# Optimization experiments

Hardware: AMD Instinct MI355X
Metric: run time of the kernel (lower is better)

## Reference

```python
import jax, jax.numpy as jnp
import numpy as np

B, N, D, H = 32, 8192, 128, 128


def setup_inputs() -> dict:
    key = jax.random.key(0)
    ks = jax.random.split(key, 9)
    s = lambda k, shp, fan: jax.random.normal(k, shp, jnp.float32) / np.sqrt(fan)
    return {
        "x": jax.random.normal(ks[0], (B, N, D), jnp.float32),
        "Wg1": s(ks[1], (D, H), D), "bg1": jnp.zeros((H,), jnp.float32),
        "Wg2": s(ks[2], (H, 1), H), "bg2": jnp.zeros((1,), jnp.float32),
        "Wn1": s(ks[3], (D, H), D), "bn1": jnp.zeros((H,), jnp.float32),
        "Wn2": s(ks[4], (H, H), H), "bn2": jnp.zeros((H,), jnp.float32),
    }


def reference(x, Wg1, bg1, Wg2, bg2, Wn1, bn1, Wn2, bn2):
    # gate_nn: Linear -> SiLU -> Linear(->1); scores per node
    gate = jnp.einsum("bnd,dh->bnh", x, Wg1) + bg1
    gate = jax.nn.silu(gate)
    gate = jnp.einsum("bnh,ho->bno", gate, Wg2) + bg2  # [B,N,1]
    # nn: Linear -> SiLU -> Linear; transformed node features
    h = jax.nn.silu(jnp.einsum("bnd,dh->bnh", x, Wn1) + bn1)
    h = jnp.einsum("bnh,hk->bnk", h, Wn2) + bn2  # [B,N,H]
    # segment softmax over nodes of each graph (segments == batch dim here)
    attn = jax.nn.softmax(gate, axis=1)  # [B,N,1]
    # weighted-sum pooling per graph
    return jnp.sum(attn * h, axis=1)  # [B,H]
```

## Files before the change

kernel.cpp:

```cpp
#include <hip/hip_runtime.h>

#define B_ 32
#define N_ 8192
#define D_ 128
#define H_ 128
#define R_ (B_ * N_)

typedef _Float16 f16;
typedef __attribute__((ext_vector_type(4))) _Float16 f16x4;
typedef __attribute__((ext_vector_type(8))) _Float16 f16x8;
typedef __attribute__((ext_vector_type(4))) float f32x4;

static constexpr size_t HWS_OFF   = 0;
static constexpr size_t WPACK_OFF = (size_t)R_ * 128 * 2;
static constexpr size_t GWS_OFF   = WPACK_OFF + 3 * 128 * 128 * 2;
static constexpr size_t MX_OFF    = GWS_OFF + (size_t)R_ * 4;
static constexpr size_t INV_OFF   = MX_OFF + 32 * 4;

__device__ __forceinline__ float silu_f(float v) {
    return v / (1.0f + __expf(-v));
}

__device__ __forceinline__ f32x4 mfma16(f16x8 a, f16x8 b, f32x4 c) {
    return __builtin_amdgcn_mfma_f32_16x16x32_f16(a, b, c, 0, 0, 0);
}

__global__ void k0_prepack(const float* __restrict__ Wg1,
                           const float* __restrict__ Wn1,
                           const float* __restrict__ Wn2,
                           f16* __restrict__ wp) {
    int tid = blockIdx.x * 256 + threadIdx.x;
    int m    = tid >> 14;
    int r    = tid & 16383;
    int j    = r & 7;
    int lane = (r >> 3) & 63;
    int kc   = (r >> 9) & 3;
    int nt   = r >> 11;
    int k = kc * 32 + (lane >> 4) * 8 + j;
    int n = nt * 16 + (lane & 15);
    const float* W = (m == 0) ? Wg1 : (m == 1) ? Wn1 : Wn2;
    wp[tid] = (f16)W[k * 128 + n];
}

__global__ __launch_bounds__(512) void k1_fused_gemm(
        const float* __restrict__ x,
        const float* __restrict__ bg1, const float* __restrict__ wg2,
        const float* __restrict__ bg2,
        const float* __restrict__ bn1, const float* __restrict__ bn2,
        const f16* __restrict__ wp,
        f16* __restrict__ hws, float* __restrict__ gws) {
    __shared__ f16 xlds[64 * 136];
    __shared__ f16 h1lds[64 * 136];
    __shared__ float gpart[8][64];

    const int tid  = threadIdx.x;
    const int w    = tid >> 6;
    const int lane = tid & 63;
    const int q    = lane >> 4;
    const int c    = lane & 15;
    const int colg = w * 16 + c;

    const f16x8* wpv = (const f16x8*)wp;
    f16x8 fg1[4], fn1[4], fn2[4];
#pragma unroll
    for (int kc = 0; kc < 4; ++kc) {
        int base = (w * 4 + kc) * 64 + lane;
        fg1[kc] = wpv[base];
        fn1[kc] = wpv[2048 + base];
        fn2[kc] = wpv[4096 + base];
    }
    const float bg1v = bg1[colg];
    const float bn1v = bn1[colg];
    const float bn2v = bn2[colg];
    const float wg2v = wg2[colg];
    const float bg2v = bg2[0];

    for (int it = 0; it < 8; ++it) {
        const long tile = (long)blockIdx.x * 8 + it;
        const long tb   = tile * 64;

        __syncthreads();

        const float4* xg = ((const float4*)x) + tb * 32;
#pragma unroll
        for (int s = 0; s < 4; ++s) {
            int i   = s * 512 + tid;
            int row = i >> 5;
            int c4  = i & 31;
            float4 v = xg[i];
            f16x4 hv = {(f16)v.x, (f16)v.y, (f16)v.z, (f16)v.w};
            *(f16x4*)&xlds[row * 136 + c4 * 4] = hv;
        }
        __syncthreads();

#pragma unroll
        for (int mt = 0; mt < 4; ++mt) {
            f16x8 a[4];
            const int arow = mt * 16 + c;
#pragma unroll
            for (int kc = 0; kc < 4; ++kc)
                a[kc] = *(const f16x8*)&xlds[arow * 136 + kc * 32 + q * 8];

            f32x4 ag = {0.f, 0.f, 0.f, 0.f};
            f32x4 an = {0.f, 0.f, 0.f, 0.f};
#pragma unroll
            for (int kc = 0; kc < 4; ++kc) {
                ag = mfma16(a[kc], fg1[kc], ag);
                an = mfma16(a[kc], fn1[kc], an);
            }
            float gp[4];
#pragma unroll
            for (int r = 0; r < 4; ++r)
                gp[r] = silu_f(ag[r] + bg1v) * wg2v;
#pragma unroll
            for (int mask = 1; mask < 16; mask <<= 1) {
#pragma unroll
                for (int r = 0; r < 4; ++r)
                    gp[r] += __shfl_xor(gp[r], mask);
            }
            if (c == 0) {
#pragma unroll
                for (int r = 0; r < 4; ++r)
                    gpart[w][mt * 16 + q * 4 + r] = gp[r];
            }
#pragma unroll
            for (int r = 0; r < 4; ++r) {
                int row = mt * 16 + q * 4 + r;
                h1lds[row * 136 + colg] = (f16)silu_f(an[r] + bn1v);
            }
        }
        __syncthreads();

        if (tid < 64) {
            float g = bg2v;
#pragma unroll
            for (int w2 = 0; w2 < 8; ++w2) g += gpart[w2][tid];
            gws[tb + tid] = g;
        }

#pragma unroll
        for (int mt = 0; mt < 4; ++mt) {
            f16x8 a[4];
            const int arow = mt * 16 + c;
#pragma unroll
            for (int kc = 0; kc < 4; ++kc)
                a[kc] = *(const f16x8*)&h1lds[arow * 136 + kc * 32 + q * 8];
            f32x4 acc = {0.f, 0.f, 0.f, 0.f};
#pragma unroll
            for (int kc = 0; kc < 4; ++kc)
                acc = mfma16(a[kc], fn2[kc], acc);
#pragma unroll
            for (int r = 0; r < 4; ++r) {
                int row = mt * 16 + q * 4 + r;
                hws[(tb + row) * 128 + colg] = (f16)(acc[r] + bn2v);
            }
        }
    }
}

__global__ void k2_softmax_stats(const float* __restrict__ gws,
                                 float* __restrict__ mx,
                                 float* __restrict__ inv,
                                 float* __restrict__ out) {
    const int b = blockIdx.x;
    const int t = threadIdx.x;
    const float* g = gws + (long)b * N_;

    float m = -1e30f;
    for (int i = t; i < N_; i += 256) m = fmaxf(m, g[i]);
#pragma unroll
    for (int mask = 1; mask < 64; mask <<= 1) m = fmaxf(m, __shfl_xor(m, mask));
    __shared__ float redm[4];
    if ((t & 63) == 0) redm[t >> 6] = m;
    __syncthreads();
    m = fmaxf(fmaxf(redm[0], redm[1]), fmaxf(redm[2], redm[3]));

    float s = 0.f;
    for (int i = t; i < N_; i += 256) s += __expf(g[i] - m);
#pragma unroll
    for (int mask = 1; mask < 64; mask <<= 1) s += __shfl_xor(s, mask);
    __shared__ float reds[4];
    if ((t & 63) == 0) reds[t >> 6] = s;
    __syncthreads();
    if (t == 0) {
        float d = reds[0] + reds[1] + reds[2] + reds[3];
        mx[b]  = m;
        inv[b] = 1.0f / d;
    }
    if (t < 128) out[b * 128 + t] = 0.f;
}

__global__ void k3_pool(const float* __restrict__ gws,
                        const f16* __restrict__ hws,
                        const float* __restrict__ mx,
                        const float* __restrict__ inv,
                        float* __restrict__ out) {
    const int ch = blockIdx.x;
    const int b  = blockIdx.y;
    const int t  = threadIdx.x;
    const long base = (long)b * N_ + (long)ch * 256;

    __shared__ float wbuf[256];
    __shared__ float part[16][128];

    wbuf[t] = __expf(gws[base + t] - mx[b]) * inv[b];
    __syncthreads();

    const int cg = t & 15;
    const int rg = t >> 4;
    const float4* hp = (const float4*)(hws + base * 128);

    float acc[8] = {0.f, 0.f, 0.f, 0.f, 0.f, 0.f, 0.f, 0.f};
#pragma unroll
    for (int r = 0; r < 16; ++r) {
        int rl = rg * 16 + r;
        float4 v = hp[rl * 16 + cg];
        float wv = wbuf[rl];
        const f16* hv = (const f16*)&v;
#pragma unroll
        for (int j = 0; j < 8; ++j) acc[j] += wv * (float)hv[j];
    }
#pragma unroll
    for (int j = 0; j < 8; ++j) part[rg][cg * 8 + j] = acc[j];
    __syncthreads();

    if (t < 128) {
        float s = 0.f;
#pragma unroll
        for (int r2 = 0; r2 < 16; ++r2) s += part[r2][t];
        atomicAdd(&out[b * 128 + t], s);
    }
}

extern "C" void kernel_launch(void* const* d_in, const int* in_sizes, int n_in,
                              void* d_out, int out_size, void* d_ws, size_t ws_size,
                              hipStream_t stream) {
    const float* x   = (const float*)d_in[0];
    const float* Wg1 = (const float*)d_in[1];
    const float* bg1 = (const float*)d_in[2];
    const float* Wg2 = (const float*)d_in[3];
    const float* bg2 = (const float*)d_in[4];
    const float* Wn1 = (const float*)d_in[5];
    const float* bn1 = (const float*)d_in[6];
    const float* Wn2 = (const float*)d_in[7];
    const float* bn2 = (const float*)d_in[8];
    float* out = (float*)d_out;

    char* ws = (char*)d_ws;
    f16*   hws = (f16*)(ws + HWS_OFF);
    f16*   wp  = (f16*)(ws + WPACK_OFF);
    float* gws = (float*)(ws + GWS_OFF);
    float* mx  = (float*)(ws + MX_OFF);
    float* inv = (float*)(ws + INV_OFF);

    k0_prepack<<<192, 256, 0, stream>>>(Wg1, Wn1, Wn2, wp);
    k1_fused_gemm<<<512, 512, 0, stream>>>(x, bg1, Wg2, bg2, bn1, bn2, wp, hws, gws);
    k2_softmax_stats<<<32, 256, 0, stream>>>(gws, mx, inv, out);
    k3_pool<<<dim3(32, 32), 256, 0, stream>>>(gws, hws, mx, inv, out);
}
```

Measured before the change: 256.1 us.

## Fuse softmax and weighted pooling into the GEMM kernel with per-block partials

```diff
diff --git a/kernel.cpp b/kernel.cpp
--- a/kernel.cpp
+++ b/kernel.cpp
@@ -11,11 +11,9 @@
 typedef __attribute__((ext_vector_type(8))) _Float16 f16x8;
 typedef __attribute__((ext_vector_type(4))) float f32x4;
 
-static constexpr size_t HWS_OFF   = 0;
-static constexpr size_t WPACK_OFF = (size_t)R_ * 128 * 2;
-static constexpr size_t GWS_OFF   = WPACK_OFF + 3 * 128 * 128 * 2;
-static constexpr size_t MX_OFF    = GWS_OFF + (size_t)R_ * 4;
-static constexpr size_t INV_OFF   = MX_OFF + 32 * 4;
+static constexpr size_t WPACK_OFF = 0;
+static constexpr size_t VPART_OFF = 98304;
+static constexpr size_t SPART_OFF = VPART_OFF + 512 * 128 * 4;
 
 __device__ __forceinline__ float silu_f(float v) {
     return v / (1.0f + __expf(-v));
@@ -42,23 +40,22 @@
     wp[tid] = (f16)W[k * 128 + n];
 }
 
-__global__ __launch_bounds__(512) void k1_fused_gemm(
+__global__ __launch_bounds__(512) void k1_fused(
         const float* __restrict__ x,
         const float* __restrict__ bg1, const float* __restrict__ wg2,
-        const float* __restrict__ bg2,
-        const float* __restrict__ bn1, const float* __restrict__ bn2,
+        const float* __restrict__ bg2, const float* __restrict__ bn1,
         const f16* __restrict__ wp,
-        f16* __restrict__ hws, float* __restrict__ gws) {
-    __shared__ f16 xlds[64 * 136];
-    __shared__ f16 h1lds[64 * 136];
+        float* __restrict__ vpart, float* __restrict__ spart) {
+    __shared__ f16 xlds[64 * 128];
+    __shared__ f16 h1lds[64 * 128];
     __shared__ float gpart[8][64];
+    __shared__ float ebuf[64];
 
     const int tid  = threadIdx.x;
     const int w    = tid >> 6;
     const int lane = tid & 63;
     const int q    = lane >> 4;
     const int c    = lane & 15;
-    const int colg = w * 16 + c;
 
     const f16x8* wpv = (const f16x8*)wp;
     f16x8 fg1[4], fn1[4], fn2[4];
@@ -69,65 +66,83 @@
         fn1[kc] = wpv[2048 + base];
         fn2[kc] = wpv[4096 + base];
     }
-    const float bg1v = bg1[colg];
-    const float bn1v = bn1[colg];
-    const float bn2v = bn2[colg];
-    const float wg2v = wg2[colg];
+    float bg1q[4], wg2q[4], bn1q[4];
+#pragma unroll
+    for (int r = 0; r < 4; ++r) {
+        int col = w * 16 + q * 4 + r;
+        bg1q[r] = bg1[col];
+        wg2q[r] = wg2[col];
+        bn1q[r] = bn1[col];
+    }
     const float bg2v = bg2[0];
 
-    for (int it = 0; it < 8; ++it) {
-        const long tile = (long)blockIdx.x * 8 + it;
-        const long tb   = tile * 64;
-
-        __syncthreads();
-
-        const float4* xg = ((const float4*)x) + tb * 32;
+    const int loh_e = (q * 16 + (c ^ q)) * 8;
+    const int loh_o = (q * 16 + (c ^ (q | 4))) * 8;
+    const int kc2 = w >> 1;
+    const int q2  = (w & 1) * 2 + (q >> 1);
+    const int v2  = ((kc2 & 1) << 2) | q2;
+    const int h1w_base = kc2 * 512 + (q2 * 16 + (c ^ v2)) * 8 + (q & 1) * 4;
+
+    float V[4] = {0.f, 0.f, 0.f, 0.f};
+    float Sl = 0.f;
+
+    const long rowbase = (long)blockIdx.x * 512;
+
+    float4 pre[4];
+    {
+        const float4* xg = (const float4*)x + rowbase * 32;
+#pragma unroll
+        for (int s = 0; s < 4; ++s) pre[s] = xg[s * 512 + tid];
+    }
+
+    for (int t = 0; t < 8; ++t) {
+        __syncthreads();
+
 #pragma unroll
         for (int s = 0; s < 4; ++s) {
-            int i   = s * 512 + tid;
-            int row = i >> 5;
-            int c4  = i & 31;
-            float4 v = xg[i];
-            f16x4 hv = {(f16)v.x, (f16)v.y, (f16)v.z, (f16)v.w};
-            *(f16x4*)&xlds[row * 136 + c4 * 4] = hv;
-        }
-        __syncthreads();
+            int e   = s * 512 + tid;
+            int row = e >> 5, c4 = e & 31;
+            int mt = row >> 4, cc = row & 15;
+            int kc = c4 >> 3, qq = (c4 >> 1) & 3, j = (c4 & 1) * 4;
+            int sw = (c4 >> 1) & 7;
+            int hidx = ((mt * 4 + kc) * 64 + qq * 16 + (cc ^ sw)) * 8 + j;
+            float4 vv = pre[s];
+            f16x4 hv = {(f16)vv.x, (f16)vv.y, (f16)vv.z, (f16)vv.w};
+            *(f16x4*)&xlds[hidx] = hv;
+        }
+        __syncthreads();
+
+        if (t < 7) {
+            const float4* xg = (const float4*)x + (rowbase + (t + 1) * 64) * 32;
+#pragma unroll
+            for (int s = 0; s < 4; ++s) pre[s] = xg[s * 512 + tid];
+        }
 
 #pragma unroll
         for (int mt = 0; mt < 4; ++mt) {
             f16x8 a[4];
-            const int arow = mt * 16 + c;
 #pragma unroll
             for (int kc = 0; kc < 4; ++kc)
-                a[kc] = *(const f16x8*)&xlds[arow * 136 + kc * 32 + q * 8];
-
+                a[kc] = *(const f16x8*)&xlds[(mt * 4 + kc) * 512 +
+                                             ((kc & 1) ? loh_o : loh_e)];
             f32x4 ag = {0.f, 0.f, 0.f, 0.f};
             f32x4 an = {0.f, 0.f, 0.f, 0.f};
 #pragma unroll
             for (int kc = 0; kc < 4; ++kc) {
-                ag = mfma16(a[kc], fg1[kc], ag);
-                an = mfma16(a[kc], fn1[kc], an);
+                ag = mfma16(fg1[kc], a[kc], ag);
+                an = mfma16(fn1[kc], a[kc], an);
             }
-            float gp[4];
+            f16x4 h4;
+#pragma unroll
+            for (int r = 0; r < 4; ++r) h4[r] = (f16)silu_f(an[r] + bn1q[r]);
+            *(f16x4*)&h1lds[mt * 2048 + h1w_base] = h4;
+            float p = 0.f;
 #pragma unroll
             for (int r = 0; r < 4; ++r)
-                gp[r] = silu_f(ag[r] + bg1v) * wg2v;
-#pragma unroll
-            for (int mask = 1; mask < 16; mask <<= 1) {
-#pragma unroll
-                for (int r = 0; r < 4; ++r)
-                    gp[r] += __shfl_xor(gp[r], mask);
-            }
-            if (c == 0) {
-#pragma unroll
-                for (int r = 0; r < 4; ++r)
-                    gpart[w][mt * 16 + q * 4 + r] = gp[r];
-            }
-#pragma unroll
-            for (int r = 0; r < 4; ++r) {
-                int row = mt * 16 + q * 4 + r;
-                h1lds[row * 136 + colg] = (f16)silu_f(an[r] + bn1v);
-            }
+                p += silu_f(ag[r] + bg1q[r]) * wg2q[r];
+            p += __shfl_xor(p, 16);
+            p += __shfl_xor(p, 32);
+            if (lane < 16) gpart[w][mt * 16 + lane] = p;
         }
         __syncthreads();
 
@@ -135,101 +150,58 @@
             float g = bg2v;
 #pragma unroll
             for (int w2 = 0; w2 < 8; ++w2) g += gpart[w2][tid];
-            gws[tb + tid] = g;
-        }
+            float e = __expf(g);
+            ebuf[tid] = e;
+            Sl += e;
+        }
+        __syncthreads();
 
 #pragma unroll
         for (int mt = 0; mt < 4; ++mt) {
-            f16x8 a[4];
-            const int arow = mt * 16 + c;
+            f16x8 b[4];
 #pragma unroll
             for (int kc = 0; kc < 4; ++kc)
-                a[kc] = *(const f16x8*)&h1lds[arow * 136 + kc * 32 + q * 8];
+                b[kc] = *(const f16x8*)&h1lds[(mt * 4 + kc) * 512 +
+                                              ((kc & 1) ? loh_o : loh_e)];
             f32x4 acc = {0.f, 0.f, 0.f, 0.f};
 #pragma unroll
             for (int kc = 0; kc < 4; ++kc)
-                acc = mfma16(a[kc], fn2[kc], acc);
-#pragma unroll
-            for (int r = 0; r < 4; ++r) {
-                int row = mt * 16 + q * 4 + r;
-                hws[(tb + row) * 128 + colg] = (f16)(acc[r] + bn2v);
-            }
-        }
-    }
-}
-
-__global__ void k2_softmax_stats(const float* __restrict__ gws,
-                                 float* __restrict__ mx,
-                                 float* __restrict__ inv,
-                                 float* __restrict__ out) {
+                acc = mfma16(fn2[kc], b[kc], acc);
+            float e = ebuf[mt * 16 + c];
+#pragma unroll
+            for (int r = 0; r < 4; ++r) V[r] += e * acc[r];
+        }
+    }
+
+#pragma unroll
+    for (int m = 1; m < 16; m <<= 1) {
+#pragma unroll
+        for (int r = 0; r < 4; ++r) V[r] += __shfl_xor(V[r], m);
+    }
+    if ((lane & 15) == 0) {
+        float4 o = {V[0], V[1], V[2], V[3]};
+        *(float4*)&vpart[(long)blockIdx.x * 128 + w * 16 + q * 4] = o;
+    }
+    if (w == 0) {
+#pragma unroll
+        for (int m = 1; m < 64; m <<= 1) Sl += __shfl_xor(Sl, m);
+        if (lane == 0) spart[blockIdx.x] = Sl;
+    }
+}
+
+__global__ void k2_combine(const float* __restrict__ vpart,
+                           const float* __restrict__ spart,
+                           const float* __restrict__ bn2,
+                           float* __restrict__ out) {
     const int b = blockIdx.x;
-    const int t = threadIdx.x;
-    const float* g = gws + (long)b * N_;
-
-    float m = -1e30f;
-    for (int i = t; i < N_; i += 256) m = fmaxf(m, g[i]);
-#pragma unroll
-    for (int mask = 1; mask < 64; mask <<= 1) m = fmaxf(m, __shfl_xor(m, mask));
-    __shared__ float redm[4];
-    if ((t & 63) == 0) redm[t >> 6] = m;
-    __syncthreads();
-    m = fmaxf(fmaxf(redm[0], redm[1]), fmaxf(redm[2], redm[3]));
-
-    float s = 0.f;
-    for (int i = t; i < N_; i += 256) s += __expf(g[i] - m);
-#pragma unroll
-    for (int mask = 1; mask < 64; mask <<= 1) s += __shfl_xor(s, mask);
-    __shared__ float reds[4];
-    if ((t & 63) == 0) reds[t >> 6] = s;
-    __syncthreads();
-    if (t == 0) {
-        float d = reds[0] + reds[1] + reds[2] + reds[3];
-        mx[b]  = m;
-        inv[b] = 1.0f / d;
-    }
-    if (t < 128) out[b * 128 + t] = 0.f;
-}
-
-__global__ void k3_pool(const float* __restrict__ gws,
-                        const f16* __restrict__ hws,
-                        const float* __restrict__ mx,
-                        const float* __restrict__ inv,
-                        float* __restrict__ out) {
-    const int ch = blockIdx.x;
-    const int b  = blockIdx.y;
-    const int t  = threadIdx.x;
-    const long base = (long)b * N_ + (long)ch * 256;
-
-    __shared__ float wbuf[256];
-    __shared__ float part[16][128];
-
-    wbuf[t] = __expf(gws[base + t] - mx[b]) * inv[b];
-    __syncthreads();
-
-    const int cg = t & 15;
-    const int rg = t >> 4;
-    const float4* hp = (const float4*)(hws + base * 128);
-
-    float acc[8] = {0.f, 0.f, 0.f, 0.f, 0.f, 0.f, 0.f, 0.f};
-#pragma unroll
-    for (int r = 0; r < 16; ++r) {
-        int rl = rg * 16 + r;
-        float4 v = hp[rl * 16 + cg];
-        float wv = wbuf[rl];
-        const f16* hv = (const f16*)&v;
-#pragma unroll
-        for (int j = 0; j < 8; ++j) acc[j] += wv * (float)hv[j];
-    }
-#pragma unroll
-    for (int j = 0; j < 8; ++j) part[rg][cg * 8 + j] = acc[j];
-    __syncthreads();
-
-    if (t < 128) {
-        float s = 0.f;
-#pragma unroll
-        for (int r2 = 0; r2 < 16; ++r2) s += part[r2][t];
-        atomicAdd(&out[b * 128 + t], s);
-    }
+    const int j = threadIdx.x;
+    float v = 0.f, s = 0.f;
+#pragma unroll
+    for (int k = 0; k < 16; ++k) {
+        v += vpart[(long)(b * 16 + k) * 128 + j];
+        s += spart[b * 16 + k];
+    }
+    out[b * 128 + j] = v / s + bn2[j];
 }
 
 extern "C" void kernel_launch(void* const* d_in, const int* in_sizes, int n_in,
@@ -247,14 +219,11 @@
     float* out = (float*)d_out;
 
     char* ws = (char*)d_ws;
-    f16*   hws = (f16*)(ws + HWS_OFF);
-    f16*   wp  = (f16*)(ws + WPACK_OFF);
-    float* gws = (float*)(ws + GWS_OFF);
-    float* mx  = (float*)(ws + MX_OFF);
-    float* inv = (float*)(ws + INV_OFF);
+    f16*   wp    = (f16*)(ws + WPACK_OFF);
+    float* vpart = (float*)(ws + VPART_OFF);
+    float* spart = (float*)(ws + SPART_OFF);
 
     k0_prepack<<<192, 256, 0, stream>>>(Wg1, Wn1, Wn2, wp);
-    k1_fused_gemm<<<512, 512, 0, stream>>>(x, bg1, Wg2, bg2, bn1, bn2, wp, hws, gws);
-    k2_softmax_stats<<<32, 256, 0, stream>>>(gws, mx, inv, out);
-    k3_pool<<<dim3(32, 32), 256, 0, stream>>>(gws, hws, mx, inv, out);
-}
+    k1_fused<<<512, 512, 0, stream>>>(x, bg1, Wg2, bg2, bn1, wp, vpart, spart);
+    k2_combine<<<32, 128, 0, stream>>>(vpart, spart, bn2, out);
+}
```

New measurement: 223.4 us. 1.15x faster.
